# Optimization experiments

Hardware: AMD Instinct MI355X
Metric: run time of the kernel (lower is better)

## Reference

```python
import jax, jax.numpy as jnp
import numpy as np

WEIGHT = 1.0


def _smooth_l1(pred, target):
    # F.smooth_l1_loss default: beta=1.0, reduction='mean'
    d = jnp.abs(pred - target)
    loss = jnp.where(d < 1.0, 0.5 * d * d, d - 0.5)
    return jnp.mean(loss)


def setup_inputs() -> dict:
    key = jax.random.key(0)
    k0, k1, k2 = jax.random.split(key, 3)
    B, L = 4096, 128
    return {
        "outputs0": jax.random.normal(k0, (B, B), dtype=jnp.float32),
        "outputs1": jax.random.normal(k1, (B, B), dtype=jnp.float32),
        "labels": jax.random.normal(k2, (B, L), dtype=jnp.float32),
    }


def reference(outputs0, outputs1, labels):
    # vector = [labels | ones]  -> [B, 2L]
    ones = jnp.ones_like(labels)
    vector = jnp.concatenate([labels, ones], axis=1)
    cos1 = vector @ vector.T                                   # [B, B]
    mod = jnp.sqrt(jnp.sum(vector * vector, axis=1, keepdims=True))  # [B, 1]
    cos2 = mod @ mod.T                                         # [B, B]
    multi_labels = jnp.floor(cos1 / cos2)                      # on-device floor (replaces cpu/numpy roundtrip)
    total_loss = (_smooth_l1(outputs0, multi_labels) + _smooth_l1(outputs1, multi_labels)) / 2.0
    return WEIGHT * total_loss
```

## Files before the change

kernel.cpp:

```cpp
#include <hip/hip_runtime.h>
#include <hip/hip_bf16.h>

#define B_N 4096
#define L_K 128
#define NPART 4096

typedef __bf16 bf16x8 __attribute__((ext_vector_type(8)));
typedef float  f32x4  __attribute__((ext_vector_type(4)));

__global__ __launch_bounds__(256) void prep_kernel(const float* __restrict__ labels,
                                                   unsigned short* __restrict__ lb,
                                                   float* __restrict__ inv) {
    const int wave = blockIdx.x * 4 + (threadIdx.x >> 6);
    const int lane = threadIdx.x & 63;
    const int row  = wave;

    const float x0 = labels[row * L_K + lane];
    const float x1 = labels[row * L_K + 64 + lane];

    __hip_bfloat16 h0 = __float2bfloat16(x0);
    __hip_bfloat16 h1 = __float2bfloat16(x1);
    lb[row * L_K + lane]      = *reinterpret_cast<unsigned short*>(&h0);
    lb[row * L_K + 64 + lane] = *reinterpret_cast<unsigned short*>(&h1);

    float s = x0 * x0 + x1 * x1;
    #pragma unroll
    for (int m = 32; m >= 1; m >>= 1) s += __shfl_xor(s, m);
    if (lane == 0) inv[row] = 1.0f / sqrtf(s + 128.0f);
}

__global__ __launch_bounds__(256) void main_kernel(const float* __restrict__ o0,
                                                   const float* __restrict__ o1,
                                                   const unsigned short* __restrict__ lb,
                                                   const float* __restrict__ inv,
                                                   float* __restrict__ partials) {
    const int w = threadIdx.x >> 6;
    const int l = threadIdx.x & 63;
    const int task = blockIdx.x * 4 + w;
    const int s = task >> 4;
    const int q = task & 15;

    const int fr = l & 15;
    const int fk = (l >> 4) * 8;
    const int r0 = s * 16;
    const int rr = (l >> 4) * 4;

    bf16x8 a[4];
    #pragma unroll
    for (int kk = 0; kk < 4; ++kk)
        a[kk] = *reinterpret_cast<const bf16x8*>(
            lb + (size_t)(r0 + fr) * L_K + kk * 32 + fk);

    float invi[4];
    #pragma unroll
    for (int r = 0; r < 4; ++r) invi[r] = inv[r0 + rr + r];

    float sumA = 0.0f, sumB = 0.0f;

    #pragma unroll
    for (int t = 0; t < 4; ++t) {
        const int c0 = q * 256 + t * 64;

        f32x4 acc[4] = {};
        #pragma unroll
        for (int kk = 0; kk < 4; ++kk) {
            #pragma unroll
            for (int ct = 0; ct < 4; ++ct) {
                const bf16x8 b = *reinterpret_cast<const bf16x8*>(
                    lb + (size_t)(c0 + ct * 16 + fr) * L_K + kk * 32 + fk);
                acc[ct] = __builtin_amdgcn_mfma_f32_16x16x32_bf16(a[kk], b, acc[ct], 0, 0, 0);
            }
        }

        float p0v[16], p1v[16];
        #pragma unroll
        for (int r = 0; r < 4; ++r) {
            const size_t rowoff = (size_t)(r0 + rr + r) * B_N + (size_t)(c0 + fr);
            #pragma unroll
            for (int ct = 0; ct < 4; ++ct) {
                p0v[r * 4 + ct] = o0[rowoff + ct * 16];
                p1v[r * 4 + ct] = o1[rowoff + ct * 16];
            }
        }

        float invj[4];
        #pragma unroll
        for (int ct = 0; ct < 4; ++ct) invj[ct] = inv[c0 + ct * 16 + fr];

        #pragma unroll
        for (int ct = 0; ct < 4; ++ct) {
            #pragma unroll
            for (int r = 0; r < 4; ++r) {
                const float m  = floorf((acc[ct][r] + 128.0f) * invi[r] * invj[ct]);
                const float d0 = fabsf(p0v[r * 4 + ct] - m);
                const float d1 = fabsf(p1v[r * 4 + ct] - m);
                const float u0 = fminf(d0, 1.0f), v0 = fmaxf(d0, 1.0f);
                const float u1 = fminf(d1, 1.0f), v1 = fmaxf(d1, 1.0f);
                sumA = fmaf(u0, u0, sumA);
                sumA = fmaf(u1, u1, sumA);
                sumB += v0 + v1;
            }
        }
    }

    float lsum = 0.5f * sumA + sumB;
    #pragma unroll
    for (int m = 32; m >= 1; m >>= 1) lsum += __shfl_xor(lsum, m);
    if (l == 0) partials[task] = lsum - 8192.0f;
}

__global__ __launch_bounds__(1024) void fin_kernel(const float* __restrict__ partials,
                                                   float* __restrict__ out) {
    __shared__ double wred[16];
    double s = 0.0;
    for (int i = threadIdx.x; i < NPART; i += 1024) s += (double)partials[i];
    #pragma unroll
    for (int m = 32; m >= 1; m >>= 1) s += __shfl_xor(s, m);
    const int l = threadIdx.x & 63, w = threadIdx.x >> 6;
    if (l == 0) wred[w] = s;
    __syncthreads();
    if (threadIdx.x == 0) {
        double t = 0.0;
        #pragma unroll
        for (int i = 0; i < 16; ++i) t += wred[i];
        out[0] = (float)(t / (2.0 * (double)B_N * (double)B_N));
    }
}

extern "C" void kernel_launch(void* const* d_in, const int* in_sizes, int n_in,
                              void* d_out, int out_size, void* d_ws, size_t ws_size,
                              hipStream_t stream) {
    const float* o0     = (const float*)d_in[0];
    const float* o1     = (const float*)d_in[1];
    const float* labels = (const float*)d_in[2];
    float* out = (float*)d_out;

    char* ws = (char*)d_ws;
    unsigned short* lb = (unsigned short*)ws;
    float* inv      = (float*)(ws + (size_t)B_N * L_K * 2);
    float* partials = (float*)(ws + (size_t)B_N * L_K * 2 + B_N * 4);

    prep_kernel<<<B_N / 4, 256, 0, stream>>>(labels, lb, inv);
    main_kernel<<<NPART / 4, 256, 0, stream>>>(o0, o1, lb, inv, partials);
    fin_kernel<<<1, 1024, 0, stream>>>(partials, out);
}
```

Baseline: 177.1 us.

## Transpose MFMA results through LDS for vectorized float4 loads of outputs

Each wave now handles one 16x64 tile instead of four, so there are four times as many tasks and partials. The two 4096x4096 output matrices are read with 16-byte vector loads in a row-contiguous layout. These loads are issued before the MFMA to hide their latency. The floored label matrix is transposed through LDS to match that layout. The cost targeted is the strided scalar global reads, which cover most of the memory-bound traffic, paid for with LDS writes and reads, a larger partials array, and a 4x larger final reduction.

Measured after the change: 169.9 us. 4.1% less time.

```diff
diff --git a/kernel.cpp b/kernel.cpp
--- a/kernel.cpp
+++ b/kernel.cpp
@@ -3,7 +3,7 @@
 
 #define B_N 4096
 #define L_K 128
-#define NPART 4096
+#define NPART 16384
 
 typedef __bf16 bf16x8 __attribute__((ext_vector_type(8)));
 typedef float  f32x4  __attribute__((ext_vector_type(4)));
@@ -34,16 +34,28 @@
                                                    const unsigned short* __restrict__ lb,
                                                    const float* __restrict__ inv,
                                                    float* __restrict__ partials) {
+    __shared__ __align__(16) float m_lds[4][16][68];
+
     const int w = threadIdx.x >> 6;
     const int l = threadIdx.x & 63;
     const int task = blockIdx.x * 4 + w;
-    const int s = task >> 4;
-    const int q = task & 15;
+    const int s = task >> 6;
+    const int c = task & 63;
 
     const int fr = l & 15;
     const int fk = (l >> 4) * 8;
+    const int g  = l >> 4;
+    const int rr = g * 4;
     const int r0 = s * 16;
-    const int rr = (l >> 4) * 4;
+    const int c0 = c * 64;
+
+    f32x4 p0[4], p1[4];
+    #pragma unroll
+    for (int v = 0; v < 4; ++v) {
+        const size_t goff = (size_t)(r0 + 4 * v + g) * B_N + (size_t)(c0 + fr * 4);
+        p0[v] = *reinterpret_cast<const f32x4*>(o0 + goff);
+        p1[v] = *reinterpret_cast<const f32x4*>(o1 + goff);
+    }
 
     bf16x8 a[4];
     #pragma unroll
@@ -51,62 +63,53 @@
         a[kk] = *reinterpret_cast<const bf16x8*>(
             lb + (size_t)(r0 + fr) * L_K + kk * 32 + fk);
 
+    f32x4 acc[4] = {};
+    #pragma unroll
+    for (int kk = 0; kk < 4; ++kk) {
+        #pragma unroll
+        for (int ct = 0; ct < 4; ++ct) {
+            const bf16x8 b = *reinterpret_cast<const bf16x8*>(
+                lb + (size_t)(c0 + ct * 16 + fr) * L_K + kk * 32 + fk);
+            acc[ct] = __builtin_amdgcn_mfma_f32_16x16x32_bf16(a[kk], b, acc[ct], 0, 0, 0);
+        }
+    }
+
     float invi[4];
     #pragma unroll
     for (int r = 0; r < 4; ++r) invi[r] = inv[r0 + rr + r];
+    float invj[4];
+    #pragma unroll
+    for (int ct = 0; ct < 4; ++ct) invj[ct] = inv[c0 + ct * 16 + fr];
+
+    #pragma unroll
+    for (int ct = 0; ct < 4; ++ct) {
+        #pragma unroll
+        for (int r = 0; r < 4; ++r) {
+            m_lds[w][rr + r][ct * 16 + fr] =
+                floorf((acc[ct][r] + 128.0f) * invi[r] * invj[ct]);
+        }
+    }
 
     float sumA = 0.0f, sumB = 0.0f;
-
     #pragma unroll
-    for (int t = 0; t < 4; ++t) {
-        const int c0 = q * 256 + t * 64;
-
-        f32x4 acc[4] = {};
+    for (int v = 0; v < 4; ++v) {
+        const f32x4 mm = *reinterpret_cast<const f32x4*>(&m_lds[w][4 * v + g][fr * 4]);
         #pragma unroll
-        for (int kk = 0; kk < 4; ++kk) {
-            #pragma unroll
-            for (int ct = 0; ct < 4; ++ct) {
-                const bf16x8 b = *reinterpret_cast<const bf16x8*>(
-                    lb + (size_t)(c0 + ct * 16 + fr) * L_K + kk * 32 + fk);
-                acc[ct] = __builtin_amdgcn_mfma_f32_16x16x32_bf16(a[kk], b, acc[ct], 0, 0, 0);
-            }
-        }
-
-        float p0v[16], p1v[16];
-        #pragma unroll
-        for (int r = 0; r < 4; ++r) {
-            const size_t rowoff = (size_t)(r0 + rr + r) * B_N + (size_t)(c0 + fr);
-            #pragma unroll
-            for (int ct = 0; ct < 4; ++ct) {
-                p0v[r * 4 + ct] = o0[rowoff + ct * 16];
-                p1v[r * 4 + ct] = o1[rowoff + ct * 16];
-            }
-        }
-
-        float invj[4];
-        #pragma unroll
-        for (int ct = 0; ct < 4; ++ct) invj[ct] = inv[c0 + ct * 16 + fr];
-
-        #pragma unroll
-        for (int ct = 0; ct < 4; ++ct) {
-            #pragma unroll
-            for (int r = 0; r < 4; ++r) {
-                const float m  = floorf((acc[ct][r] + 128.0f) * invi[r] * invj[ct]);
-                const float d0 = fabsf(p0v[r * 4 + ct] - m);
-                const float d1 = fabsf(p1v[r * 4 + ct] - m);
-                const float u0 = fminf(d0, 1.0f), v0 = fmaxf(d0, 1.0f);
-                const float u1 = fminf(d1, 1.0f), v1 = fmaxf(d1, 1.0f);
-                sumA = fmaf(u0, u0, sumA);
-                sumA = fmaf(u1, u1, sumA);
-                sumB += v0 + v1;
-            }
+        for (int q = 0; q < 4; ++q) {
+            const float d0 = fabsf(p0[v][q] - mm[q]);
+            const float d1 = fabsf(p1[v][q] - mm[q]);
+            const float u0 = fminf(d0, 1.0f), v0 = fmaxf(d0, 1.0f);
+            const float u1 = fminf(d1, 1.0f), v1 = fmaxf(d1, 1.0f);
+            sumA = fmaf(u0, u0, sumA);
+            sumA = fmaf(u1, u1, sumA);
+            sumB += v0 + v1;
         }
     }
 
     float lsum = 0.5f * sumA + sumB;
     #pragma unroll
     for (int m = 32; m >= 1; m >>= 1) lsum += __shfl_xor(lsum, m);
-    if (l == 0) partials[task] = lsum - 8192.0f;
+    if (l == 0) partials[task] = lsum - 2048.0f;
 }
 
 __global__ __launch_bounds__(1024) void fin_kernel(const float* __restrict__ partials,
```
